# Performance work log

Hardware: AMD Instinct MI355X
Metric: run time of the kernel (lower is better)

Reference implementation:

```python
import jax, jax.numpy as jnp
import numpy as np

H, D = 8, 16
NA, NB, E, F = 50000, 50000, 200000, 128
SQRT_D = float(np.sqrt(D))


def _proj(x, W, b):
    # Linear then split heads: [N, F] -> [N, H, D]
    return (x @ W + b).reshape(x.shape[0], H, D)


def _seg_softmax(alpha, idx, n):
    # softmax over edges sharing the same destination node (per head)
    amax = jax.ops.segment_max(alpha, idx, num_segments=n)
    amax = jnp.where(jnp.isfinite(amax), amax, 0.0)
    ex = jnp.exp(alpha - amax[idx])
    den = jax.ops.segment_sum(ex, idx, num_segments=n)
    return ex / (den[idx] + 1e-16)


def _hgt_conv(xa, xb, eis, Wk, bk, Wq, bq, Wv, bv, Wa, ba, skip, arel, mrel, prel):
    # node types: 0='a', 1='b'; edge types: 0 a->b, 1 b->a, 2 a->a
    xs = (xa, xb)
    k = [_proj(xs[t], Wk[t], bk[t]) for t in range(2)]
    q = [_proj(xs[t], Wq[t], bq[t]) for t in range(2)]
    v = [_proj(xs[t], Wv[t], bv[t]) for t in range(2)]
    nn_ = (xa.shape[0], xb.shape[0])
    agg = [jnp.zeros((nn_[t], H, D), xa.dtype) for t in range(2)]
    spec = ((0, 1, eis[0]), (1, 0, eis[1]), (0, 0, eis[2]))
    for e, (s, d, ei) in enumerate(spec):
        src, dst = ei[0], ei[1]
        k_rel = jnp.einsum('nhd,hde->nhe', k[s], arel[e])  # [Ns,H,D]
        v_rel = jnp.einsum('nhd,hde->nhe', v[s], mrel[e])
        alpha = jnp.sum(q[d][dst] * k_rel[src], axis=-1) * prel[e] / SQRT_D  # [E,H]
        w = _seg_softmax(alpha, dst, nn_[d])
        agg[d] = agg[d] + jax.ops.segment_sum(v_rel[src] * w[..., None], dst, num_segments=nn_[d])
    outs = []
    for t in range(2):
        o = jax.nn.gelu(agg[t].reshape(-1, H * D), approximate=False) @ Wa[t] + ba[t]
        sgate = jax.nn.sigmoid(skip[t])  # learned skip-gate, dims match so always applied
        outs.append(sgate * o + (1.0 - sgate) * xs[t])
    return outs[0], outs[1]


def _forward(xa, xb, eis, Wk, bk, Wq, bq, Wv, bv, Wa, ba, skip, arel, mrel, prel):
    for l in range(2):
        xa, xb = _hgt_conv(xa, xb, eis, Wk[l], bk[l], Wq[l], bq[l], Wv[l], bv[l],
                           Wa[l], ba[l], skip[l], arel[l], mrel[l], prel[l])
        if l < 1:
            xa, xb = jax.nn.relu(xa), jax.nn.relu(xb)  # dropout: identity in eval mode
    return xa, xb


def setup_inputs() -> dict:
    key = jax.random.key(0)
    ks = jax.random.split(key, 12)
    s = 0.05
    return {
        'xa': jax.random.normal(ks[0], (NA, F), jnp.float32),
        'xb': jax.random.normal(ks[1], (NB, F), jnp.float32),
        'ei_ab': jax.random.randint(ks[2], (2, E), 0, NA, dtype=jnp.int32),
        'ei_ba': jax.random.randint(ks[3], (2, E), 0, NB, dtype=jnp.int32),
        'ei_aa': jax.random.randint(ks[4], (2, E), 0, NA, dtype=jnp.int32),
        'Wk': jax.random.normal(ks[5], (2, 2, F, F), jnp.float32) * s,
        'bk': jnp.zeros((2, 2, F), jnp.float32),
        'Wq': jax.random.normal(ks[6], (2, 2, F, F), jnp.float32) * s,
        'bq': jnp.zeros((2, 2, F), jnp.float32),
        'Wv': jax.random.normal(ks[7], (2, 2, F, F), jnp.float32) * s,
        'bv': jnp.zeros((2, 2, F), jnp.float32),
        'Wa': jax.random.normal(ks[8], (2, 2, F, F), jnp.float32) * s,
        'ba': jnp.zeros((2, 2, F), jnp.float32),
        'skip': jnp.zeros((2, 2), jnp.float32),
        'arel': jax.random.normal(ks[9], (2, 3, H, D, D), jnp.float32) * (1.0 / SQRT_D),
        'mrel': jax.random.normal(ks[10], (2, 3, H, D, D), jnp.float32) * (1.0 / SQRT_D),
        'prel': jnp.ones((2, 3, H), jnp.float32),
    }


def reference(xa, xb, ei_ab, ei_ba, ei_aa, Wk, bk, Wq, bq, Wv, bv, Wa, ba, skip, arel, mrel, prel):
    return _forward(xa, xb, (ei_ab, ei_ba, ei_aa), Wk, bk, Wq, bq, Wv, bv, Wa, ba, skip, arel, mrel, prel)
```

## Files before the change

### kernel.cpp

```cpp
#include <hip/hip_runtime.h>
#include <hip/hip_bf16.h>
#include <math.h>

#define F 128
#define NH 8
#define HD 16

static inline int cdiv(int a, int b) { return (a + b - 1) / b; }

typedef __attribute__((ext_vector_type(8))) short bf16x8;
typedef __attribute__((ext_vector_type(4))) float f32x4;

__device__ __forceinline__ float geluf(float x) {
    return 0.5f * x * (1.f + erff(x * 0.70710678118654752440f));
}

__device__ __forceinline__ short f2bf(float f) {
    __hip_bfloat16 h = __float2bfloat16(f);
    return *reinterpret_cast<short*>(&h);
}

__device__ __forceinline__ float bflo(unsigned int u) { return __uint_as_float(u << 16); }
__device__ __forceinline__ float bfhi(unsigned int u) { return __uint_as_float(u & 0xffff0000u); }
__device__ __forceinline__ float bf2f(short s) {
    return __uint_as_float(((unsigned int)(unsigned short)s) << 16);
}
__device__ __forceinline__ unsigned int packbf(float a, float b) {
    return (unsigned int)(unsigned short)f2bf(a) | ((unsigned int)(unsigned short)f2bf(b) << 16);
}

__device__ __forceinline__ void slot_info(int slot, int& kind, int& wsel, int& e, int& t) {
    switch (slot) {
        case 0: kind = 0; wsel = 0; t = 0; e = 0; break;
        case 1: kind = 1; wsel = 1; t = 0; e = 0; break;
        case 2: kind = 1; wsel = 2; t = 0; e = 0; break;
        case 3: kind = 1; wsel = 1; t = 0; e = 2; break;
        case 4: kind = 1; wsel = 2; t = 0; e = 2; break;
        case 5: kind = 0; wsel = 0; t = 1; e = 0; break;
        case 6: kind = 1; wsel = 1; t = 1; e = 1; break;
        case 7: kind = 1; wsel = 2; t = 1; e = 1; break;
        case 8: kind = 0; wsel = 3; t = 0; e = 0; break;
        default: kind = 0; wsel = 3; t = 1; e = 0; break;
    }
}

__global__ void prep_weights(const float* __restrict__ Wk, const float* __restrict__ bk,
                             const float* __restrict__ Wq, const float* __restrict__ bq,
                             const float* __restrict__ Wv, const float* __restrict__ bv,
                             const float* __restrict__ Wa, const float* __restrict__ ba,
                             const float* __restrict__ arel, const float* __restrict__ mrel,
                             short* __restrict__ Wslots, float* __restrict__ bslots) {
    const int WTOT = 10 * 16384;
    const int layer = blockIdx.y;
    short* Wl = Wslots + (size_t)layer * WTOT;
    float* bl = bslots + (size_t)layer * 10 * 128;
    int idx = blockIdx.x * blockDim.x + threadIdx.x;
    if (idx < WTOT) {
        int slot = idx >> 14, rem = idx & 16383;
        int n = rem >> 7, k = rem & 127;
        int kind, wsel, e, t;
        slot_info(slot, kind, wsel, e, t);
        float out;
        if (kind == 0) {
            const float* Wb = (wsel == 0 ? Wq : Wa) + (size_t)(layer * 2 + t) * 16384;
            out = Wb[k * 128 + n];
        } else {
            int h = n >> 4, j = n & 15;
            const float* Wb = (wsel == 1 ? Wk : Wv) + (size_t)(layer * 2 + t) * 16384;
            const float* R = (wsel == 1 ? arel : mrel) + (size_t)((layer * 3 + e) * NH + h) * 256;
            float s = 0.f;
            #pragma unroll
            for (int d = 0; d < HD; ++d) s += Wb[k * 128 + h * 16 + d] * R[d * 16 + j];
            out = s;
        }
        Wl[(size_t)slot * 16384 + n * 128 + k] = f2bf(out);
    } else {
        int r = idx - WTOT;
        if (r < 10 * 128) {
            int slot = r >> 7, n = r & 127;
            int kind, wsel, e, t;
            slot_info(slot, kind, wsel, e, t);
            float out;
            if (kind == 0) {
                const float* bb = (wsel == 0 ? bq : ba) + (size_t)(layer * 2 + t) * 128;
                out = bb[n];
            } else {
                int h = n >> 4, j = n & 15;
                const float* bb = (wsel == 1 ? bk : bv) + (size_t)(layer * 2 + t) * 128;
                const float* R = (wsel == 1 ? arel : mrel) + (size_t)((layer * 3 + e) * NH + h) * 256;
                float s = 0.f;
                #pragma unroll
                for (int d = 0; d < HD; ++d) s += bb[h * 16 + d] * R[d * 16 + j];
                out = s;
            }
            bl[slot * 128 + n] = out;
        }
    }
}

__device__ __forceinline__ short* qkv_slot_ptr(int side, int s,
    short* qA, short* kA0, short* vA0, short* kA2, short* vA2,
    short* qB, short* kB1, short* vB1) {
    if (side) {
        if (s == 0) return qB;
        if (s == 1) return kB1;
        return vB1;
    }
    if (s == 0) return qA;
    if (s == 1) return kA0;
    if (s == 2) return vA0;
    if (s == 3) return kA2;
    return vA2;
}

__global__ __launch_bounds__(256) void gemm_qkv_all(
    const float* __restrict__ Aa, const float* __restrict__ Ab,
    const short* __restrict__ Wl, const float* __restrict__ bl,
    short* __restrict__ qA, short* __restrict__ kA0, short* __restrict__ vA0,
    short* __restrict__ kA2, short* __restrict__ vA2,
    short* __restrict__ qB, short* __restrict__ kB1, short* __restrict__ vB1,
    int NA_, int NB_, int nbA) {
    __shared__ short Ws[128 * 136];
    __shared__ short As[64 * 136];
    float* Wsf = (float*)Ws;
    const int tid = threadIdx.x;
    const int bid = blockIdx.x;
    const int side = bid >= nbA;
    const float* A = side ? Ab : Aa;
    const int N = side ? NB_ : NA_;
    const int row0 = (side ? bid - nbA : bid) * 64;
    const short* Wbase = Wl + (side ? (size_t)5 * 16384 : 0);
    const float* bbase = bl + (side ? 5 * 128 : 0);
    const int S = side ? 3 : 5;

    #pragma unroll
    for (int it = 0; it < 4; ++it) {
        int chunk = tid + it * 256;
        int r = chunk >> 4, c8 = (chunk & 15) * 8;
        int gr = row0 + r;
        bf16x8 s = {};
        if (gr < N) {
            float4 v0 = *(const float4*)&A[(size_t)gr * F + c8];
            float4 v1 = *(const float4*)&A[(size_t)gr * F + c8 + 4];
            s[0] = f2bf(v0.x); s[1] = f2bf(v0.y); s[2] = f2bf(v0.z); s[3] = f2bf(v0.w);
            s[4] = f2bf(v1.x); s[5] = f2bf(v1.y); s[6] = f2bf(v1.z); s[7] = f2bf(v1.w);
        }
        *(bf16x8*)&As[r * 136 + c8] = s;
    }
    __syncthreads();

    const int wave = tid >> 6;
    const int lane = tid & 63;
    const int m16 = lane & 15;
    const int kg = lane >> 4;
    const int arow = wave * 16 + m16;

    bf16x8 af[4];
    #pragma unroll
    for (int kq = 0; kq < 4; ++kq)
        af[kq] = *(const bf16x8*)&As[arow * 136 + kq * 32 + kg * 8];

    for (int s = 0; s < S; ++s) {
        if (s) __syncthreads();
        const short* Wt = Wbase + (size_t)s * 16384;
        #pragma unroll
        for (int it = 0; it < 8; ++it) {
            int chunk = tid + it * 256;
            int r = chunk >> 4, c8 = (chunk & 15) * 8;
            *(int4*)&Ws[r * 136 + c8] = *(const int4*)&Wt[r * 128 + c8];
        }
        __syncthreads();

        f32x4 acc[8] = {};
        #pragma unroll
        for (int kq = 0; kq < 4; ++kq) {
            #pragma unroll
            for (int nt = 0; nt < 8; ++nt) {
                bf16x8 b = *(const bf16x8*)&Ws[(nt * 16 + m16) * 136 + kq * 32 + kg * 8];
                acc[nt] = __builtin_amdgcn_mfma_f32_16x16x32_bf16(af[kq], b, acc[nt], 0, 0, 0);
            }
        }
        __syncthreads();

        #pragma unroll
        for (int nt = 0; nt < 8; ++nt)
            #pragma unroll
            for (int r = 0; r < 4; ++r)
                Wsf[(wave * 16 + kg * 4 + r) * 132 + nt * 16 + m16] = acc[nt][r];
        __syncthreads();

        short* optr = qkv_slot_ptr(side, s, qA, kA0, vA0, kA2, vA2, qB, kB1, vB1);
        const float* bias = bbase + s * 128;
        #pragma unroll
        for (int it = 0; it < 4; ++it) {
            int chunk = tid + it * 256;
            int r = chunk >> 4, c8 = (chunk & 15) * 8;
            int gr = row0 + r;
            if (gr >= N) continue;
            float4 b0 = *(const float4*)&bias[c8];
            float4 b1 = *(const float4*)&bias[c8 + 4];
            bf16x8 o;
            o[0] = f2bf(Wsf[r * 132 + c8 + 0] + b0.x);
            o[1] = f2bf(Wsf[r * 132 + c8 + 1] + b0.y);
            o[2] = f2bf(Wsf[r * 132 + c8 + 2] + b0.z);
            o[3] = f2bf(Wsf[r * 132 + c8 + 3] + b0.w);
            o[4] = f2bf(Wsf[r * 132 + c8 + 4] + b1.x);
            o[5] = f2bf(Wsf[r * 132 + c8 + 5] + b1.y);
            o[6] = f2bf(Wsf[r * 132 + c8 + 6] + b1.z);
            o[7] = f2bf(Wsf[r * 132 + c8 + 7] + b1.w);
            *(bf16x8*)&optr[(size_t)gr * F + c8] = o;
        }
    }
}

__global__ __launch_bounds__(256) void fused_out_qkv(
    const short* __restrict__ aggA, const short* __restrict__ aggB,
    const short* __restrict__ Wl0, const float* __restrict__ bl0,
    const float* __restrict__ xfA, const float* __restrict__ xfB,
    const float* __restrict__ skipp,
    const short* __restrict__ Wl1, const float* __restrict__ bl1,
    short* __restrict__ x1A, short* __restrict__ x1B,
    short* __restrict__ qA, short* __restrict__ kA0, short* __restrict__ vA0,
    short* __restrict__ kA2, short* __restrict__ vA2,
    short* __restrict__ qB, short* __restrict__ kB1, short* __restrict__ vB1,
    int NA_, int NB_, int nbA) {
    __shared__ short Ws[128 * 136];
    __shared__ short As[64 * 136];
    float* Wsf = (float*)Ws;
    const int tid = threadIdx.x;
    const int bid = blockIdx.x;
    const int side = bid >= nbA;
    const short* A = side ? aggB : aggA;
    const int N = side ? NB_ : NA_;
    const int row0 = (side ? bid - nbA : bid) * 64;
    const short* Wt0 = Wl0 + (size_t)(side ? 9 : 8) * 16384;
    const float* bias0 = bl0 + (side ? 9 : 8) * 128;

    #pragma unroll
    for (int it = 0; it < 8; ++it) {
        int chunk = tid + it * 256;
        int r = chunk >> 4, c8 = (chunk & 15) * 8;
        *(int4*)&Ws[r * 136 + c8] = *(const int4*)&Wt0[r * 128 + c8];
    }
    #pragma unroll
    for (int it = 0; it < 4; ++it) {
        int chunk = tid + it * 256;
        int r = chunk >> 4, c8 = (chunk & 15) * 8;
        int gr = row0 + r;
        bf16x8 s = {};
        if (gr < N) {
            s = *(const bf16x8*)&A[(size_t)gr * F + c8];
            #pragma unroll
            for (int u = 0; u < 8; ++u) s[u] = f2bf(geluf(bf2f(s[u])));
        }
        *(bf16x8*)&As[r * 136 + c8] = s;
    }
    __syncthreads();

    const int wave = tid >> 6;
    const int lane = tid & 63;
    const int m16 = lane & 15;
    const int kgv = lane >> 4;
    const int arow = wave * 16 + m16;

    {
        f32x4 acc[8] = {};
        #pragma unroll
        for (int k0 = 0; k0 < 128; k0 += 32) {
            bf16x8 a = *(const bf16x8*)&As[arow * 136 + k0 + kgv * 8];
            #pragma unroll
            for (int nt = 0; nt < 8; ++nt) {
                bf16x8 b = *(const bf16x8*)&Ws[(nt * 16 + m16) * 136 + k0 + kgv * 8];
                acc[nt] = __builtin_amdgcn_mfma_f32_16x16x32_bf16(a, b, acc[nt], 0, 0, 0);
            }
        }
        __syncthreads();
        #pragma unroll
        for (int nt = 0; nt < 8; ++nt)
            #pragma unroll
            for (int r = 0; r < 4; ++r)
                Wsf[(wave * 16 + kgv * 4 + r) * 132 + nt * 16 + m16] = acc[nt][r];
        __syncthreads();
    }

    {
        float sg = 1.f / (1.f + expf(-skipp[side]));
        short* x1 = side ? x1B : x1A;
        const float* xf = side ? xfB : xfA;
        #pragma unroll
        for (int it = 0; it < 4; ++it) {
            int chunk = tid + it * 256;
            int r = chunk >> 4, c8 = (chunk & 15) * 8;
            int gr = row0 + r;
            if (gr >= N) continue;
            float4 b0 = *(const float4*)&bias0[c8];
            float4 b1 = *(const float4*)&bias0[c8 + 4];
            float4 x0v = *(const float4*)&xf[(size_t)gr * F + c8];
            float4 x1v = *(const float4*)&xf[(size_t)gr * F + c8 + 4];
            float v[8];
            #pragma unroll
            for (int u = 0; u < 8; ++u) v[u] = Wsf[r * 132 + c8 + u];
            v[0] += b0.x; v[1] += b0.y; v[2] += b0.z; v[3] += b0.w;
            v[4] += b1.x; v[5] += b1.y; v[6] += b1.z; v[7] += b1.w;
            float xr[8] = {x0v.x, x0v.y, x0v.z, x0v.w, x1v.x, x1v.y, x1v.z, x1v.w};
            bf16x8 o;
            #pragma unroll
            for (int u = 0; u < 8; ++u)
                o[u] = f2bf(fmaxf(sg * v[u] + (1.f - sg) * xr[u], 0.f));
            *(bf16x8*)&x1[(size_t)gr * F + c8] = o;
            *(bf16x8*)&As[r * 136 + c8] = o;
        }
    }
    __syncthreads();

    bf16x8 af[4];
    #pragma unroll
    for (int kq = 0; kq < 4; ++kq)
        af[kq] = *(const bf16x8*)&As[arow * 136 + kq * 32 + kgv * 8];

    const short* Wbase = Wl1 + (side ? (size_t)5 * 16384 : 0);
    const float* bbase = bl1 + (side ? 5 * 128 : 0);
    const int S = side ? 3 : 5;

    for (int s = 0; s < S; ++s) {
        __syncthreads();
        const short* Wt = Wbase + (size_t)s * 16384;
        #pragma unroll
        for (int it = 0; it < 8; ++it) {
            int chunk = tid + it * 256;
            int r = chunk >> 4, c8 = (chunk & 15) * 8;
            *(int4*)&Ws[r * 136 + c8] = *(const int4*)&Wt[r * 128 + c8];
        }
        __syncthreads();

        f32x4 acc[8] = {};
        #pragma unroll
        for (int kq = 0; kq < 4; ++kq) {
            #pragma unroll
            for (int nt = 0; nt < 8; ++nt) {
                bf16x8 b = *(const bf16x8*)&Ws[(nt * 16 + m16) * 136 + kq * 32 + kgv * 8];
                acc[nt] = __builtin_amdgcn_mfma_f32_16x16x32_bf16(af[kq], b, acc[nt], 0, 0, 0);
            }
        }
        __syncthreads();

        #pragma unroll
        for (int nt = 0; nt < 8; ++nt)
            #pragma unroll
            for (int r = 0; r < 4; ++r)
                Wsf[(wave * 16 + kgv * 4 + r) * 132 + nt * 16 + m16] = acc[nt][r];
        __syncthreads();

        short* optr = qkv_slot_ptr(side, s, qA, kA0, vA0, kA2, vA2, qB, kB1, vB1);
        const float* bias = bbase + s * 128;
        #pragma unroll
        for (int it = 0; it < 4; ++it) {
            int chunk = tid + it * 256;
            int r = chunk >> 4, c8 = (chunk & 15) * 8;
            int gr = row0 + r;
            if (gr >= N) continue;
            float4 b0 = *(const float4*)&bias[c8];
            float4 b1 = *(const float4*)&bias[c8 + 4];
            bf16x8 o;
            o[0] = f2bf(Wsf[r * 132 + c8 + 0] + b0.x);
            o[1] = f2bf(Wsf[r * 132 + c8 + 1] + b0.y);
            o[2] = f2bf(Wsf[r * 132 + c8 + 2] + b0.z);
            o[3] = f2bf(Wsf[r * 132 + c8 + 3] + b0.w);
            o[4] = f2bf(Wsf[r * 132 + c8 + 4] + b1.x);
            o[5] = f2bf(Wsf[r * 132 + c8 + 5] + b1.y);
            o[6] = f2bf(Wsf[r * 132 + c8 + 6] + b1.z);
            o[7] = f2bf(Wsf[r * 132 + c8 + 7] + b1.w);
            *(bf16x8*)&optr[(size_t)gr * F + c8] = o;
        }
    }
}

__global__ __launch_bounds__(256) void gemm_out_final(
    const short* __restrict__ aggA, const short* __restrict__ aggB,
    const short* __restrict__ Wl, const float* __restrict__ bl,
    const short* __restrict__ xbA, const short* __restrict__ xbB,
    const float* __restrict__ skipp,
    float* __restrict__ CfA, float* __restrict__ CfB,
    int NA_, int NB_, int nbA) {
    __shared__ short Ws[128 * 136];
    __shared__ short As[64 * 136];
    float* Wsf = (float*)Ws;
    const int tid = threadIdx.x;
    const int bid = blockIdx.x;
    const int side = bid >= nbA;
    const short* A = side ? aggB : aggA;
    const int N = side ? NB_ : NA_;
    const int row0 = (side ? bid - nbA : bid) * 64;
    const short* Wt = Wl + (size_t)(side ? 9 : 8) * 16384;
    const float* bias = bl + (side ? 9 : 8) * 128;

    #pragma unroll
    for (int it = 0; it < 8; ++it) {
        int chunk = tid + it * 256;
        int r = chunk >> 4, c8 = (chunk & 15) * 8;
        *(int4*)&Ws[r * 136 + c8] = *(const int4*)&Wt[r * 128 + c8];
    }
    #pragma unroll
    for (int it = 0; it < 4; ++it) {
        int chunk = tid + it * 256;
        int r = chunk >> 4, c8 = (chunk & 15) * 8;
        int gr = row0 + r;
        bf16x8 s = {};
        if (gr < N) {
            s = *(const bf16x8*)&A[(size_t)gr * F + c8];
            #pragma unroll
            for (int u = 0; u < 8; ++u) s[u] = f2bf(geluf(bf2f(s[u])));
        }
        *(bf16x8*)&As[r * 136 + c8] = s;
    }
    __syncthreads();

    const int wave = tid >> 6;
    const int lane = tid & 63;
    const int m16 = lane & 15;
    const int kg = lane >> 4;
    const int arow = wave * 16 + m16;

    f32x4 acc[8] = {};
    #pragma unroll
    for (int k0 = 0; k0 < 128; k0 += 32) {
        bf16x8 a = *(const bf16x8*)&As[arow * 136 + k0 + kg * 8];
        #pragma unroll
        for (int nt = 0; nt < 8; ++nt) {
            bf16x8 b = *(const bf16x8*)&Ws[(nt * 16 + m16) * 136 + k0 + kg * 8];
            acc[nt] = __builtin_amdgcn_mfma_f32_16x16x32_bf16(a, b, acc[nt], 0, 0, 0);
        }
    }
    __syncthreads();

    #pragma unroll
    for (int nt = 0; nt < 8; ++nt)
        #pragma unroll
        for (int r = 0; r < 4; ++r)
            Wsf[(wave * 16 + kg * 4 + r) * 132 + nt * 16 + m16] = acc[nt][r];
    __syncthreads();

    float sg = 1.f / (1.f + expf(-skipp[side]));
    #pragma unroll
    for (int it = 0; it < 4; ++it) {
        int chunk = tid + it * 256;
        int r = chunk >> 4, c8 = (chunk & 15) * 8;
        int gr = row0 + r;
        if (gr >= N) continue;
        float4 b0 = *(const float4*)&bias[c8];
        float4 b1 = *(const float4*)&bias[c8 + 4];
        float v[8];
        #pragma unroll
        for (int u = 0; u < 8; ++u) v[u] = Wsf[r * 132 + c8 + u];
        v[0] += b0.x; v[1] += b0.y; v[2] += b0.z; v[3] += b0.w;
        v[4] += b1.x; v[5] += b1.y; v[6] += b1.z; v[7] += b1.w;
        const short* xb = side ? xbB : xbA;
        bf16x8 xrv = *(const bf16x8*)&xb[(size_t)gr * F + c8];
        float* Cf = side ? CfB : CfA;
        float o[8];
        #pragma unroll
        for (int u = 0; u < 8; ++u)
            o[u] = sg * v[u] + (1.f - sg) * bf2f(xrv[u]);
        *(float4*)&Cf[(size_t)gr * F + c8]     = make_float4(o[0], o[1], o[2], o[3]);
        *(float4*)&Cf[(size_t)gr * F + c8 + 4] = make_float4(o[4], o[5], o[6], o[7]);
    }
}


__global__ void hist_all(const int* __restrict__ ei0, const int* __restrict__ ei1,
                         const int* __restrict__ ei2, int E0, int E1, int E2,
                         int NB_, int NA_, int* __restrict__ cnt) {
    int i = blockIdx.x * 256 + threadIdx.x;
    if (i >= E0 + E1 + E2) return;
    const int* ei; int li, Ee, base;
    if (i < E0)           { li = i;           ei = ei0; Ee = E0; base = 0; }
    else if (i < E0 + E1) { li = i - E0;      ei = ei1; Ee = E1; base = NB_; }
    else                  { li = i - E0 - E1; ei = ei2; Ee = E2; base = NB_ + NA_; }
    atomicAdd(&cnt[base + ei[Ee + li]], 1);
}

__global__ void scan1(const int* __restrict__ cnt, int n, int* __restrict__ off,
                      int* __restrict__ bsum) {
    __shared__ int lds[256];
    int tid = threadIdx.x, i = blockIdx.x * 256 + tid;
    int v = (i < n) ? cnt[i] : 0;
    lds[tid] = v;
    __syncthreads();
    #pragma unroll
    for (int s = 1; s < 256; s <<= 1) {
        int t = (tid >= s) ? lds[tid - s] : 0;
        __syncthreads();
        lds[tid] += t;
        __syncthreads();
    }
    if (i < n) off[i] = lds[tid] - v;
    if (tid == 255) bsum[blockIdx.x] = lds[255];
}

__global__ __launch_bounds__(1024) void scan2(int* __restrict__ bsum, int nb,
                                              int* __restrict__ off_n) {
    __shared__ int lds[1024];
    int tid = threadIdx.x;
    int v = (tid < nb) ? bsum[tid] : 0;
    lds[tid] = v;
    __syncthreads();
    #pragma unroll
    for (int s = 1; s < 1024; s <<= 1) {
        int t = (tid >= s) ? lds[tid - s] : 0;
        __syncthreads();
        lds[tid] += t;
        __syncthreads();
    }
    if (tid < nb) bsum[tid] = lds[tid] - v;
    if (tid == 1023) *off_n = lds[1023];
}

__global__ void scan3(int* __restrict__ off, int* __restrict__ woff,
                      const int* __restrict__ bsum, int n) {
    int i = blockIdx.x * 256 + threadIdx.x;
    if (i < n) {
        int v = off[i] + bsum[blockIdx.x];
        off[i] = v;
        woff[i] = v;
    }
}

__global__ void scatter_all(const int* __restrict__ ei0, const int* __restrict__ ei1,
                            const int* __restrict__ ei2, int E0, int E1, int E2,
                            int NB_, int NA_, int* __restrict__ woff,
                            int* __restrict__ csr_src) {
    int i = blockIdx.x * 256 + threadIdx.x;
    if (i >= E0 + E1 + E2) return;
    const int* ei; int li, Ee, base;
    if (i < E0)           { li = i;           ei = ei0; Ee = E0; base = 0; }
    else if (i < E0 + E1) { li = i - E0;      ei = ei1; Ee = E1; base = NB_; }
    else                  { li = i - E0 - E1; ei = ei2; Ee = E2; base = NB_ + NA_; }
    int p = atomicAdd(&woff[base + ei[Ee + li]], 1);
    csr_src[p] = ei[li] * 16;
}

__device__ __forceinline__ void seg_set4(
    const uint4* __restrict__ kArr, const uint4* __restrict__ vArr,
    int c0, int e1, const int* __restrict__ csr, int s, int p,
    const float* __restrict__ qf, float pr,
    float* __restrict__ accv, float& den) {
    for (; c0 < e1; c0 += 4) {
        int rem = e1 - c0;
        bool act = s < rem;
        int sj = csr[c0 + (act ? s : 0)];
        uint4 kw = kArr[sj + p];
        uint4 vw = vArr[sj + p];
        float d = bflo(kw.x) * qf[0];
        d = fmaf(bfhi(kw.x), qf[1], d);
        d = fmaf(bflo(kw.y), qf[2], d);
        d = fmaf(bfhi(kw.y), qf[3], d);
        d = fmaf(bflo(kw.z), qf[4], d);
        d = fmaf(bfhi(kw.z), qf[5], d);
        d = fmaf(bflo(kw.w), qf[6], d);
        d = fmaf(bfhi(kw.w), qf[7], d);
        d += __shfl_xor(d, 1);
        float ex = __expf(fminf(d * pr, 80.f));
        ex = act ? ex : 0.f;
        den += ex;
        accv[0] = fmaf(ex, bflo(vw.x), accv[0]);
        accv[1] = fmaf(ex, bfhi(vw.x), accv[1]);
        accv[2] = fmaf(ex, bflo(vw.y), accv[2]);
        accv[3] = fmaf(ex, bfhi(vw.y), accv[3]);
        accv[4] = fmaf(ex, bflo(vw.z), accv[4]);
        accv[5] = fmaf(ex, bfhi(vw.z), accv[5]);
        accv[6] = fmaf(ex, bflo(vw.w), accv[6]);
        accv[7] = fmaf(ex, bfhi(vw.w), accv[7]);
    }
}

__device__ __forceinline__ void seg_fold(float* __restrict__ accv, float& den,
                                         float* __restrict__ r) {
    #pragma unroll
    for (int j = 0; j < 8; ++j) {
        accv[j] += __shfl_xor(accv[j], 16);
        accv[j] += __shfl_xor(accv[j], 32);
    }
    den += __shfl_xor(den, 16);
    den += __shfl_xor(den, 32);
    float inv = 1.f / (den + 1e-16f);
    #pragma unroll
    for (int j = 0; j < 8; ++j) r[j] = fmaf(accv[j], inv, r[j]);
}

__global__ __launch_bounds__(256) void seg_attn_all(
    const short* __restrict__ qA, const short* __restrict__ kA0,
    const short* __restrict__ vA0, const short* __restrict__ kA2,
    const short* __restrict__ vA2, const short* __restrict__ qB,
    const short* __restrict__ kB1, const short* __restrict__ vB1,
    const int* __restrict__ off0, const int* __restrict__ off1,
    const int* __restrict__ off2, const int* __restrict__ csrS,
    const float* __restrict__ prelL,
    short* __restrict__ aggA, short* __restrict__ aggB,
    int NA_, int NB_, int nba) {
    const int wv = threadIdx.x >> 6;
    const int l = threadIdx.x & 63;
    const int s = l >> 4;
    const int p = l & 15;
    const int h = p >> 1;
    const int isA = (int)blockIdx.x < nba;
    int dst = (isA ? blockIdx.x : blockIdx.x - nba) * 4 + wv;
    if (dst >= (isA ? NA_ : NB_)) return;

    uint4 qw = ((const uint4*)(isA ? qA : qB))[(size_t)dst * 16 + p];
    float qf[8] = {bflo(qw.x), bfhi(qw.x), bflo(qw.y), bfhi(qw.y),
                   bflo(qw.z), bfhi(qw.z), bflo(qw.w), bfhi(qw.w)};

    float r[8] = {};
    float accv[8] = {};
    float den = 0.f;
    if (isA) {
        seg_set4((const uint4*)kB1, (const uint4*)vB1, off1[dst], off1[dst + 1],
                 csrS, s, p, qf, prelL[1 * NH + h] * 0.25f, accv, den);
        seg_fold(accv, den, r);
        #pragma unroll
        for (int j = 0; j < 8; ++j) accv[j] = 0.f;
        den = 0.f;
        seg_set4((const uint4*)kA2, (const uint4*)vA2, off2[dst], off2[dst + 1],
                 csrS, s, p, qf, prelL[2 * NH + h] * 0.25f, accv, den);
        seg_fold(accv, den, r);
    } else {
        seg_set4((const uint4*)kA0, (const uint4*)vA0, off0[dst], off0[dst + 1],
                 csrS, s, p, qf, prelL[0 * NH + h] * 0.25f, accv, den);
        seg_fold(accv, den, r);
    }
    if (s == 0) {
        uint4 o;
        o.x = packbf(r[0], r[1]);
        o.y = packbf(r[2], r[3]);
        o.z = packbf(r[4], r[5]);
        o.w = packbf(r[6], r[7]);
        ((uint4*)(isA ? aggA : aggB))[(size_t)dst * 16 + p] = o;
    }
}

extern "C" void kernel_launch(void* const* d_in, const int* in_sizes, int n_in,
                              void* d_out, int out_size, void* d_ws, size_t ws_size,
                              hipStream_t stream) {
    const float* xa   = (const float*)d_in[0];
    const float* xb   = (const float*)d_in[1];
    const int* ei_ab  = (const int*)d_in[2];
    const int* ei_ba  = (const int*)d_in[3];
    const int* ei_aa  = (const int*)d_in[4];
    const float* Wk   = (const float*)d_in[5];
    const float* bk   = (const float*)d_in[6];
    const float* Wq   = (const float*)d_in[7];
    const float* bq   = (const float*)d_in[8];
    const float* Wv   = (const float*)d_in[9];
    const float* bv   = (const float*)d_in[10];
    const float* Wa   = (const float*)d_in[11];
    const float* ba   = (const float*)d_in[12];
    const float* skip = (const float*)d_in[13];
    const float* arel = (const float*)d_in[14];
    const float* mrel = (const float*)d_in[15];
    const float* prel = (const float*)d_in[16];

    const int NA = in_sizes[0] / F;
    const int NB = in_sizes[1] / F;
    const int E0 = in_sizes[2] / 2, E1 = in_sizes[3] / 2, E2 = in_sizes[4] / 2;
    const int ET = E0 + E1 + E2;
    const int NT = NB + NA + NA;

    float* ws = (float*)d_ws;
    size_t o = 0;
    float* bslots = ws + o; o += 2 * 10 * 128;
    int* iws = (int*)(ws + o);
    size_t io = 0;
    int* cnt   = iws + io; io += NT;
    int* bsum  = iws + io; io += 1024;
    int* offc  = iws + io; io += NT + 1;
    int* woff  = iws + io; io += NT;
    int* csrS  = iws + io; io += ET;
    io = (io + 7) & ~(size_t)7;
    short* sws = (short*)(iws + io);
    size_t so = 0;
    short* qA  = sws + so; so += (size_t)NA * 128;
    short* kA0 = sws + so; so += (size_t)NA * 128;
    short* vA0 = sws + so; so += (size_t)NA * 128;
    short* kA2 = sws + so; so += (size_t)NA * 128;
    short* vA2 = sws + so; so += (size_t)NA * 128;
    short* qB  = sws + so; so += (size_t)NB * 128;
    short* kB1 = sws + so; so += (size_t)NB * 128;
    short* vB1 = sws + so; so += (size_t)NB * 128;
    short* aggA = sws + so; so += (size_t)NA * 128;
    short* aggB = sws + so; so += (size_t)NB * 128;
    short* x1ab = sws + so; so += (size_t)NA * 128;
    short* x1bb = sws + so; so += (size_t)NB * 128;
    short* Wslots = sws + so; so += (size_t)2 * 10 * 16384;

    float* outA = (float*)d_out;
    float* outB = (float*)d_out + (size_t)NA * F;

    {
        dim3 g(cdiv(10 * 16384 + 10 * 128, 256), 2);
        prep_weights<<<g, 256, 0, stream>>>(Wk, bk, Wq, bq, Wv, bv, Wa, ba,
                                            arel, mrel, Wslots, bslots);
    }

    hipMemsetAsync(cnt, 0, (size_t)NT * sizeof(int), stream);
    hist_all<<<cdiv(ET, 256), 256, 0, stream>>>(ei_ab, ei_ba, ei_aa, E0, E1, E2, NB, NA, cnt);
    {
        int nb = cdiv(NT, 256);
        scan1<<<nb, 256, 0, stream>>>(cnt, NT, offc, bsum);
        scan2<<<1, 1024, 0, stream>>>(bsum, nb, offc + NT);
        scan3<<<nb, 256, 0, stream>>>(offc, woff, bsum, NT);
    }
    scatter_all<<<cdiv(ET, 256), 256, 0, stream>>>(ei_ab, ei_ba, ei_aa, E0, E1, E2, NB, NA, woff, csrS);

    const int* off_e0 = offc;
    const int* off_e1 = offc + NB;
    const int* off_e2 = offc + NB + NA;

    const int nbA64 = cdiv(NA, 64), nbB64 = cdiv(NB, 64);
    const int nba4 = cdiv(NA, 4), nbb4 = cdiv(NB, 4);

    const short* Wl0 = Wslots;
    const short* Wl1 = Wslots + (size_t)10 * 16384;
    const float* bl0 = bslots;
    const float* bl1 = bslots + 10 * 128;

    gemm_qkv_all<<<nbA64 + nbB64, 256, 0, stream>>>(
        xa, xb, Wl0, bl0, qA, kA0, vA0, kA2, vA2, qB, kB1, vB1, NA, NB, nbA64);

    seg_attn_all<<<nba4 + nbb4, 256, 0, stream>>>(
        qA, kA0, vA0, kA2, vA2, qB, kB1, vB1,
        off_e0, off_e1, off_e2, csrS, prel, aggA, aggB, NA, NB, nba4);

    fused_out_qkv<<<nbA64 + nbB64, 256, 0, stream>>>(
        aggA, aggB, Wl0, bl0, xa, xb, skip, Wl1, bl1,
        x1ab, x1bb, qA, kA0, vA0, kA2, vA2, qB, kB1, vB1, NA, NB, nbA64);

    seg_attn_all<<<nba4 + nbb4, 256, 0, stream>>>(
        qA, kA0, vA0, kA2, vA2, qB, kB1, vB1,
        off_e0, off_e1, off_e2, csrS, prel + 3 * NH, aggA, aggB, NA, NB, nba4);

    gemm_out_final<<<nbA64 + nbB64, 256, 0, stream>>>(
        aggA, aggB, Wl1, bl1, x1ab, x1bb, skip + 2, outA, outB, NA, NB, nbA64);
}
```

Before: 341.2 us.

## Stage GEMM weights via direct global-to-LDS loads with XOR-free rotated swizzle

The prep kernel now stores the bf16 weight tiles with a per-row rotation of 16-byte chunks. The GEMM kernels then copy them straight into LDS with global_load_lds (16-byte) instead of going through registers with a padded layout. B-fragment reads use the matching rotated index so they avoid bank conflicts without padding, and epilogue LDS reads become float4 vector loads. This cuts register traffic and instruction count when staging weights. The cost is a tighter coupling between the prep layout and the consumers, plus a dependence on the direct LDS-load builtin.

```diff
diff --git a/kernel.cpp b/kernel.cpp
--- a/kernel.cpp
+++ b/kernel.cpp
@@ -27,6 +27,12 @@
 }
 __device__ __forceinline__ unsigned int packbf(float a, float b) {
     return (unsigned int)(unsigned short)f2bf(a) | ((unsigned int)(unsigned short)f2bf(b) << 16);
+}
+
+__device__ __forceinline__ void glds16(const void* g, void* l) {
+    __builtin_amdgcn_global_load_lds(
+        (const __attribute__((address_space(1))) unsigned int*)g,
+        (__attribute__((address_space(3))) unsigned int*)l, 16, 0, 0);
 }
 
 __device__ __forceinline__ void slot_info(int slot, int& kind, int& wsel, int& e, int& t) {
@@ -73,7 +79,9 @@
             for (int d = 0; d < HD; ++d) s += Wb[k * 128 + h * 16 + d] * R[d * 16 + j];
             out = s;
         }
-        Wl[(size_t)slot * 16384 + n * 128 + k] = f2bf(out);
+        int chunk = k >> 3, kin = k & 7;
+        int cph = (chunk + (n & 15)) & 15;
+        Wl[(size_t)slot * 16384 + n * 128 + cph * 8 + kin] = f2bf(out);
     } else {
         int r = idx - WTOT;
         if (r < 10 * 128) {
@@ -113,6 +121,15 @@
     return vA2;
 }
 
+__device__ __forceinline__ void stage_W(const short* __restrict__ Wt, short* Ws,
+                                        int wave, int lane) {
+    #pragma unroll
+    for (int it = 0; it < 8; ++it) {
+        int off = (it * 4 + wave) * 1024;
+        glds16((const char*)Wt + off + lane * 16, (char*)Ws + off);
+    }
+}
+
 __global__ __launch_bounds__(256) void gemm_qkv_all(
     const float* __restrict__ Aa, const float* __restrict__ Ab,
     const short* __restrict__ Wl, const float* __restrict__ bl,
@@ -120,9 +137,9 @@
     short* __restrict__ kA2, short* __restrict__ vA2,
     short* __restrict__ qB, short* __restrict__ kB1, short* __restrict__ vB1,
     int NA_, int NB_, int nbA) {
-    __shared__ short Ws[128 * 136];
-    __shared__ short As[64 * 136];
-    float* Wsf = (float*)Ws;
+    __shared__ __align__(16) float Wsf[64 * 132];
+    __shared__ __align__(16) short As[64 * 136];
+    short* Ws = (short*)Wsf;
     const int tid = threadIdx.x;
     const int bid = blockIdx.x;
     const int side = bid >= nbA;
@@ -132,6 +149,12 @@
     const short* Wbase = Wl + (side ? (size_t)5 * 16384 : 0);
     const float* bbase = bl + (side ? 5 * 128 : 0);
     const int S = side ? 3 : 5;
+
+    const int wave = tid >> 6;
+    const int lane = tid & 63;
+    const int m16 = lane & 15;
+    const int kg = lane >> 4;
+    const int arow = wave * 16 + m16;
 
     #pragma unroll
     for (int it = 0; it < 4; ++it) {
@@ -149,12 +172,6 @@
     }
     __syncthreads();
 
-    const int wave = tid >> 6;
-    const int lane = tid & 63;
-    const int m16 = lane & 15;
-    const int kg = lane >> 4;
-    const int arow = wave * 16 + m16;
-
     bf16x8 af[4];
     #pragma unroll
     for (int kq = 0; kq < 4; ++kq)
@@ -162,13 +179,7 @@
 
     for (int s = 0; s < S; ++s) {
         if (s) __syncthreads();
-        const short* Wt = Wbase + (size_t)s * 16384;
-        #pragma unroll
-        for (int it = 0; it < 8; ++it) {
-            int chunk = tid + it * 256;
-            int r = chunk >> 4, c8 = (chunk & 15) * 8;
-            *(int4*)&Ws[r * 136 + c8] = *(const int4*)&Wt[r * 128 + c8];
-        }
+        stage_W(Wbase + (size_t)s * 16384, Ws, wave, lane);
         __syncthreads();
 
         f32x4 acc[8] = {};
@@ -176,7 +187,8 @@
         for (int kq = 0; kq < 4; ++kq) {
             #pragma unroll
             for (int nt = 0; nt < 8; ++nt) {
-                bf16x8 b = *(const bf16x8*)&Ws[(nt * 16 + m16) * 136 + kq * 32 + kg * 8];
+                int cph = (kq * 4 + kg + m16) & 15;
+                bf16x8 b = *(const bf16x8*)&Ws[(nt * 16 + m16) * 128 + cph * 8];
                 acc[nt] = __builtin_amdgcn_mfma_f32_16x16x32_bf16(af[kq], b, acc[nt], 0, 0, 0);
             }
         }
@@ -199,15 +211,13 @@
             if (gr >= N) continue;
             float4 b0 = *(const float4*)&bias[c8];
             float4 b1 = *(const float4*)&bias[c8 + 4];
+            float4 va = *(float4*)&Wsf[r * 132 + c8];
+            float4 vb = *(float4*)&Wsf[r * 132 + c8 + 4];
             bf16x8 o;
-            o[0] = f2bf(Wsf[r * 132 + c8 + 0] + b0.x);
-            o[1] = f2bf(Wsf[r * 132 + c8 + 1] + b0.y);
-            o[2] = f2bf(Wsf[r * 132 + c8 + 2] + b0.z);
-            o[3] = f2bf(Wsf[r * 132 + c8 + 3] + b0.w);
-            o[4] = f2bf(Wsf[r * 132 + c8 + 4] + b1.x);
-            o[5] = f2bf(Wsf[r * 132 + c8 + 5] + b1.y);
-            o[6] = f2bf(Wsf[r * 132 + c8 + 6] + b1.z);
-            o[7] = f2bf(Wsf[r * 132 + c8 + 7] + b1.w);
+            o[0] = f2bf(va.x + b0.x); o[1] = f2bf(va.y + b0.y);
+            o[2] = f2bf(va.z + b0.z); o[3] = f2bf(va.w + b0.w);
+            o[4] = f2bf(vb.x + b1.x); o[5] = f2bf(vb.y + b1.y);
+            o[6] = f2bf(vb.z + b1.z); o[7] = f2bf(vb.w + b1.w);
             *(bf16x8*)&optr[(size_t)gr * F + c8] = o;
         }
     }
@@ -224,9 +234,9 @@
     short* __restrict__ kA2, short* __restrict__ vA2,
     short* __restrict__ qB, short* __restrict__ kB1, short* __restrict__ vB1,
     int NA_, int NB_, int nbA) {
-    __shared__ short Ws[128 * 136];
-    __shared__ short As[64 * 136];
-    float* Wsf = (float*)Ws;
+    __shared__ __align__(16) float Wsf[64 * 132];
+    __shared__ __align__(16) short As[64 * 136];
+    short* Ws = (short*)Wsf;
     const int tid = threadIdx.x;
     const int bid = blockIdx.x;
     const int side = bid >= nbA;
@@ -236,12 +246,13 @@
     const short* Wt0 = Wl0 + (size_t)(side ? 9 : 8) * 16384;
     const float* bias0 = bl0 + (side ? 9 : 8) * 128;
 
-    #pragma unroll
-    for (int it = 0; it < 8; ++it) {
-        int chunk = tid + it * 256;
-        int r = chunk >> 4, c8 = (chunk & 15) * 8;
-        *(int4*)&Ws[r * 136 + c8] = *(const int4*)&Wt0[r * 128 + c8];
-    }
+    const int wave = tid >> 6;
+    const int lane = tid & 63;
+    const int m16 = lane & 15;
+    const int kg = lane >> 4;
+    const int arow = wave * 16 + m16;
+
+    stage_W(Wt0, Ws, wave, lane);
     #pragma unroll
     for (int it = 0; it < 4; ++it) {
         int chunk = tid + it * 256;
@@ -257,20 +268,15 @@
     }
     __syncthreads();
 
-    const int wave = tid >> 6;
-    const int lane = tid & 63;
-    const int m16 = lane & 15;
-    const int kgv = lane >> 4;
-    const int arow = wave * 16 + m16;
-
     {
         f32x4 acc[8] = {};
         #pragma unroll
-        for (int k0 = 0; k0 < 128; k0 += 32) {
-            bf16x8 a = *(const bf16x8*)&As[arow * 136 + k0 + kgv * 8];
+        for (int kq = 0; kq < 4; ++kq) {
+            bf16x8 a = *(const bf16x8*)&As[arow * 136 + kq * 32 + kg * 8];
             #pragma unroll
             for (int nt = 0; nt < 8; ++nt) {
-                bf16x8 b = *(const bf16x8*)&Ws[(nt * 16 + m16) * 136 + k0 + kgv * 8];
+                int cph = (kq * 4 + kg + m16) & 15;
+                bf16x8 b = *(const bf16x8*)&Ws[(nt * 16 + m16) * 128 + cph * 8];
                 acc[nt] = __builtin_amdgcn_mfma_f32_16x16x32_bf16(a, b, acc[nt], 0, 0, 0);
             }
         }
@@ -279,7 +285,7 @@
         for (int nt = 0; nt < 8; ++nt)
             #pragma unroll
             for (int r = 0; r < 4; ++r)
-                Wsf[(wave * 16 + kgv * 4 + r) * 132 + nt * 16 + m16] = acc[nt][r];
+                Wsf[(wave * 16 + kg * 4 + r) * 132 + nt * 16 + m16] = acc[nt][r];
         __syncthreads();
     }
 
@@ -295,13 +301,12 @@
             if (gr >= N) continue;
             float4 b0 = *(const float4*)&bias0[c8];
             float4 b1 = *(const float4*)&bias0[c8 + 4];
+            float4 va = *(float4*)&Wsf[r * 132 + c8];
+            float4 vb = *(float4*)&Wsf[r * 132 + c8 + 4];
             float4 x0v = *(const float4*)&xf[(size_t)gr * F + c8];
             float4 x1v = *(const float4*)&xf[(size_t)gr * F + c8 + 4];
-            float v[8];
-            #pragma unroll
-            for (int u = 0; u < 8; ++u) v[u] = Wsf[r * 132 + c8 + u];
-            v[0] += b0.x; v[1] += b0.y; v[2] += b0.z; v[3] += b0.w;
-            v[4] += b1.x; v[5] += b1.y; v[6] += b1.z; v[7] += b1.w;
+            float v[8] = {va.x + b0.x, va.y + b0.y, va.z + b0.z, va.w + b0.w,
+                          vb.x + b1.x, vb.y + b1.y, vb.z + b1.z, vb.w + b1.w};
             float xr[8] = {x0v.x, x0v.y, x0v.z, x0v.w, x1v.x, x1v.y, x1v.z, x1v.w};
             bf16x8 o;
             #pragma unroll
@@ -316,7 +321,7 @@
     bf16x8 af[4];
     #pragma unroll
     for (int kq = 0; kq < 4; ++kq)
-        af[kq] = *(const bf16x8*)&As[arow * 136 + kq * 32 + kgv * 8];
+        af[kq] = *(const bf16x8*)&As[arow * 136 + kq * 32 + kg * 8];
 
     const short* Wbase = Wl1 + (side ? (size_t)5 * 16384 : 0);
     const float* bbase = bl1 + (side ? 5 * 128 : 0);
@@ -324,13 +329,7 @@
 
     for (int s = 0; s < S; ++s) {
         __syncthreads();
-        const short* Wt = Wbase + (size_t)s * 16384;
-        #pragma unroll
-        for (int it = 0; it < 8; ++it) {
-            int chunk = tid + it * 256;
-            int r = chunk >> 4, c8 = (chunk & 15) * 8;
-            *(int4*)&Ws[r * 136 + c8] = *(const int4*)&Wt[r * 128 + c8];
-        }
+        stage_W(Wbase + (size_t)s * 16384, Ws, wave, lane);
         __syncthreads();
 
         f32x4 acc[8] = {};
@@ -338,7 +337,8 @@
         for (int kq = 0; kq < 4; ++kq) {
             #pragma unroll
             for (int nt = 0; nt < 8; ++nt) {
-                bf16x8 b = *(const bf16x8*)&Ws[(nt * 16 + m16) * 136 + kq * 32 + kgv * 8];
+                int cph = (kq * 4 + kg + m16) & 15;
+                bf16x8 b = *(const bf16x8*)&Ws[(nt * 16 + m16) * 128 + cph * 8];
                 acc[nt] = __builtin_amdgcn_mfma_f32_16x16x32_bf16(af[kq], b, acc[nt], 0, 0, 0);
             }
         }
@@ -348,7 +348,7 @@
         for (int nt = 0; nt < 8; ++nt)
             #pragma unroll
             for (int r = 0; r < 4; ++r)
-                Wsf[(wave * 16 + kgv * 4 + r) * 132 + nt * 16 + m16] = acc[nt][r];
+                Wsf[(wave * 16 + kg * 4 + r) * 132 + nt * 16 + m16] = acc[nt][r];
         __syncthreads();
 
         short* optr = qkv_slot_ptr(side, s, qA, kA0, vA0, kA2, vA2, qB, kB1, vB1);
@@ -361,15 +361,13 @@
             if (gr >= N) continue;
             float4 b0 = *(const float4*)&bias[c8];
             float4 b1 = *(const float4*)&bias[c8 + 4];
+            float4 va = *(float4*)&Wsf[r * 132 + c8];
+            float4 vb = *(float4*)&Wsf[r * 132 + c8 + 4];
             bf16x8 o;
-            o[0] = f2bf(Wsf[r * 132 + c8 + 0] + b0.x);
-            o[1] = f2bf(Wsf[r * 132 + c8 + 1] + b0.y);
-            o[2] = f2bf(Wsf[r * 132 + c8 + 2] + b0.z);
-            o[3] = f2bf(Wsf[r * 132 + c8 + 3] + b0.w);
-            o[4] = f2bf(Wsf[r * 132 + c8 + 4] + b1.x);
-            o[5] = f2bf(Wsf[r * 132 + c8 + 5] + b1.y);
-            o[6] = f2bf(Wsf[r * 132 + c8 + 6] + b1.z);
-            o[7] = f2bf(Wsf[r * 132 + c8 + 7] + b1.w);
+            o[0] = f2bf(va.x + b0.x); o[1] = f2bf(va.y + b0.y);
+            o[2] = f2bf(va.z + b0.z); o[3] = f2bf(va.w + b0.w);
+            o[4] = f2bf(vb.x + b1.x); o[5] = f2bf(vb.y + b1.y);
+            o[6] = f2bf(vb.z + b1.z); o[7] = f2bf(vb.w + b1.w);
             *(bf16x8*)&optr[(size_t)gr * F + c8] = o;
         }
     }
@@ -382,9 +380,9 @@
     const float* __restrict__ skipp,
     float* __restrict__ CfA, float* __restrict__ CfB,
     int NA_, int NB_, int nbA) {
-    __shared__ short Ws[128 * 136];
-    __shared__ short As[64 * 136];
-    float* Wsf = (float*)Ws;
+    __shared__ __align__(16) float Wsf[64 * 132];
+    __shared__ __align__(16) short As[64 * 136];
+    short* Ws = (short*)Wsf;
     const int tid = threadIdx.x;
     const int bid = blockIdx.x;
     const int side = bid >= nbA;
@@ -394,12 +392,13 @@
     const short* Wt = Wl + (size_t)(side ? 9 : 8) * 16384;
     const float* bias = bl + (side ? 9 : 8) * 128;
 
-    #pragma unroll
-    for (int it = 0; it < 8; ++it) {
-        int chunk = tid + it * 256;
-        int r = chunk >> 4, c8 = (chunk & 15) * 8;
-        *(int4*)&Ws[r * 136 + c8] = *(const int4*)&Wt[r * 128 + c8];
-    }
+    const int wave = tid >> 6;
+    const int lane = tid & 63;
+    const int m16 = lane & 15;
+    const int kg = lane >> 4;
+    const int arow = wave * 16 + m16;
+
+    stage_W(Wt, Ws, wave, lane);
     #pragma unroll
     for (int it = 0; it < 4; ++it) {
         int chunk = tid + it * 256;
@@ -415,19 +414,14 @@
     }
     __syncthreads();
 
-    const int wave = tid >> 6;
-    const int lane = tid & 63;
-    const int m16 = lane & 15;
-    const int kg = lane >> 4;
-    const int arow = wave * 16 + m16;
-
     f32x4 acc[8] = {};
     #pragma unroll
-    for (int k0 = 0; k0 < 128; k0 += 32) {
-        bf16x8 a = *(const bf16x8*)&As[arow * 136 + k0 + kg * 8];
+    for (int kq = 0; kq < 4; ++kq) {
+        bf16x8 a = *(const bf16x8*)&As[arow * 136 + kq * 32 + kg * 8];
         #pragma unroll
         for (int nt = 0; nt < 8; ++nt) {
-            bf16x8 b = *(const bf16x8*)&Ws[(nt * 16 + m16) * 136 + k0 + kg * 8];
+            int cph = (kq * 4 + kg + m16) & 15;
+            bf16x8 b = *(const bf16x8*)&Ws[(nt * 16 + m16) * 128 + cph * 8];
             acc[nt] = __builtin_amdgcn_mfma_f32_16x16x32_bf16(a, b, acc[nt], 0, 0, 0);
         }
     }
@@ -449,11 +443,10 @@
         if (gr >= N) continue;
         float4 b0 = *(const float4*)&bias[c8];
         float4 b1 = *(const float4*)&bias[c8 + 4];
-        float v[8];
-        #pragma unroll
-        for (int u = 0; u < 8; ++u) v[u] = Wsf[r * 132 + c8 + u];
-        v[0] += b0.x; v[1] += b0.y; v[2] += b0.z; v[3] += b0.w;
-        v[4] += b1.x; v[5] += b1.y; v[6] += b1.z; v[7] += b1.w;
+        float4 va = *(float4*)&Wsf[r * 132 + c8];
+        float4 vb = *(float4*)&Wsf[r * 132 + c8 + 4];
+        float v[8] = {va.x + b0.x, va.y + b0.y, va.z + b0.z, va.w + b0.w,
+                      vb.x + b1.x, vb.y + b1.y, vb.z + b1.z, vb.w + b1.w};
         const short* xb = side ? xbB : xbA;
         bf16x8 xrv = *(const bf16x8*)&xb[(size_t)gr * F + c8];
         float* Cf = side ? CfB : CfA;
```

Measured after the change: 335.7 us. Within noise of the previous version (-1.6%).
